# Performance work log

Measured on AMD Instinct MI355X. Metric: run time of the kernel, lower is better.

## Reference

```python
import jax, jax.numpy as jnp
import numpy as np

EMBED_DIM = 2048
NUM_HEADS = 32
HEAD_DIM = EMBED_DIM // NUM_HEADS  # 64
SCALE = HEAD_DIM ** -0.5


def setup_inputs() -> dict:
    key = jax.random.key(0)
    k1, k2, k3, k4, k5 = jax.random.split(key, 5)
    B, S, D = 1, 2048, EMBED_DIM
    return {
        "hidden_states": jax.random.normal(k1, (B, S, D), jnp.float32),
        "w_qkv": jax.random.normal(k2, (3 * D, D), jnp.float32) * (D ** -0.5),
        "b_qkv": jax.random.normal(k3, (3 * D,), jnp.float32) * 0.02,
        "w_out": jax.random.normal(k4, (D, D), jnp.float32) * (D ** -0.5),
        "b_out": jax.random.normal(k5, (D,), jnp.float32) * 0.02,
    }


def reference(hidden_states, w_qkv, b_qkv, w_out, b_out):
    B, S, D = hidden_states.shape
    H, Hd = NUM_HEADS, HEAD_DIM
    # fused QKV projection: [B,S,3D]
    qkv = jnp.einsum("bsd,ed->bse", hidden_states, w_qkv) + b_qkv
    q, k, v = jnp.split(qkv, 3, axis=-1)
    # [B,H,S,Hd]
    q = q.reshape(B, S, H, Hd).transpose(0, 2, 1, 3)
    k = k.reshape(B, S, H, Hd).transpose(0, 2, 1, 3)
    v = v.reshape(B, S, H, Hd).transpose(0, 2, 1, 3)
    scores = jnp.einsum("bhqd,bhkd->bhqk", q, k) * SCALE
    causal = jnp.tril(jnp.ones((S, S), bool))  # [S,S]
    scores = jnp.where(causal, scores, jnp.finfo(scores.dtype).min)
    probs = jax.nn.softmax(scores, axis=-1)
    attn = jnp.einsum("bhqk,bhkd->bhqd", probs, v)
    attn = attn.transpose(0, 2, 1, 3).reshape(B, S, D)
    return jnp.einsum("bsd,ed->bse", attn, w_out) + b_out
```

## Files before the change

kernel.cpp:

```cpp
#include <hip/hip_runtime.h>
#include <hip/hip_bf16.h>

typedef __bf16 bf16;
typedef __attribute__((ext_vector_type(8))) __bf16 bf16x8;
typedef __attribute__((ext_vector_type(4))) float f32x4;

#define S_LEN 2048
#define DM 2048
#define NH 32
#define HD 64
#define QKV_LD 6144
#define SCALE2 0.18033688011112042f
#define DEFER_THR 8.0f

__device__ __forceinline__ float fast_exp2(float x) {
  return __builtin_amdgcn_exp2f(x);
}

__device__ __forceinline__ void gload_lds16(const bf16* g, const bf16* l) {
  __builtin_amdgcn_global_load_lds(
      (const __attribute__((address_space(1))) void*)(uintptr_t)g,
      (__attribute__((address_space(3))) void*)(uint32_t)(uintptr_t)l,
      16, 0, 0);
}

template <int N>
__device__ __forceinline__ void waitcnt_vm() {
  if constexpr (N == 0)      asm volatile("s_waitcnt vmcnt(0)" ::: "memory");
  else if constexpr (N == 4) asm volatile("s_waitcnt vmcnt(4)" ::: "memory");
  else if constexpr (N == 5) asm volatile("s_waitcnt vmcnt(5)" ::: "memory");
  else if constexpr (N == 6) asm volatile("s_waitcnt vmcnt(6)" ::: "memory");
  else if constexpr (N == 7) asm volatile("s_waitcnt vmcnt(7)" ::: "memory");
  else if constexpr (N == 8) asm volatile("s_waitcnt vmcnt(8)" ::: "memory");
  else static_assert(N == 0, "add vmcnt case");
}

template <int CTRL>
__device__ __forceinline__ float fdpp(float x) {
  return __builtin_bit_cast(float,
      __builtin_amdgcn_update_dpp(0, __builtin_bit_cast(int, x), CTRL, 0xF, 0xF, true));
}
__device__ __forceinline__ float red16_max(float x) {
  x = fmaxf(x, fdpp<0xB1>(x));
  x = fmaxf(x, fdpp<0x4E>(x));
  x = fmaxf(x, fdpp<0x141>(x));
  x = fmaxf(x, fdpp<0x140>(x));
  return x;
}
__device__ __forceinline__ float red16_sum(float x) {
  x += fdpp<0xB1>(x);
  x += fdpp<0x4E>(x);
  x += fdpp<0x141>(x);
  x += fdpp<0x140>(x);
  return x;
}

__global__ __launch_bounds__(256) void cvt3_f32_bf16(
    const float* __restrict__ s0, bf16* __restrict__ d0, const int n0,
    const float* __restrict__ s1, bf16* __restrict__ d1, const int n1,
    const float* __restrict__ s2, bf16* __restrict__ d2, const int n2)
{
  const int total = n0 + n1 + n2;
  const int stride = gridDim.x * blockDim.x;
  for (int i = blockIdx.x * blockDim.x + threadIdx.x; i < total; i += stride) {
    const float* s; bf16* d; int j = i;
    if (j < n0)            { s = s0; d = d0; }
    else if (j - n0 < n1)  { s = s1; d = d1; j -= n0; }
    else                   { s = s2; d = d2; j -= n0 + n1; }
    const f32x4 a = *(const f32x4*)(s + (size_t)j * 8);
    const f32x4 b = *(const f32x4*)(s + (size_t)j * 8 + 4);
    bf16x8 r;
    r[0] = (bf16)a[0]; r[1] = (bf16)a[1]; r[2] = (bf16)a[2]; r[3] = (bf16)a[3];
    r[4] = (bf16)b[0]; r[5] = (bf16)b[1]; r[6] = (bf16)b[2]; r[7] = (bf16)b[3];
    *(bf16x8*)(d + (size_t)j * 8) = r;
  }
}

template <int BM, int BN, int WRN, int WCN, int NT, int MINW, typename TO>
__global__ __launch_bounds__(NT, MINW) void gemm_pipe(
    const bf16* __restrict__ A, const bf16* __restrict__ W,
    const float* __restrict__ bias, TO* __restrict__ C,
    const int M, const int N, const int K)
{
  constexpr int WM = BM / WRN, WN = BN / WCN;
  constexpr int MI = WM / 16, NI = WN / 16;
  constexpr int CA = (BM * 64 * 2) / (NT * 16);
  constexpr int CB = (BN * 64 * 2) / (NT * 16);
  constexpr int BUFE = (BM + BN) * 64;
  __shared__ __align__(16) bf16 lds[2 * BUFE];
  const int tid  = threadIdx.x;
  const int lane = tid & 63;
  const int wid  = tid >> 6;
  const int wr = wid / WCN, wc = wid % WCN;
  const int row0 = blockIdx.y * BM, col0 = blockIdx.x * BN;
  const int lq = lane & 15, seg = lane >> 4;

  const f32x4 fz = {0.f, 0.f, 0.f, 0.f};
  f32x4 acc[MI][NI];
#pragma unroll
  for (int i = 0; i < MI; ++i)
#pragma unroll
    for (int j = 0; j < NI; ++j) acc[i][j] = fz;

  auto stage = [&](const int kt, const int b) {
    const int k0 = kt << 6;
    bf16* Ab = lds + b * BUFE;
    bf16* Bb = Ab + BM * 64;
#pragma unroll
    for (int c = 0; c < CA; ++c) {
      const int off16 = c * NT + tid;
      const int row = off16 >> 3;
      const int ch  = (off16 & 7) ^ (row & 7);
      gload_lds16(A + (size_t)(row0 + row) * K + k0 + (ch << 3),
                  Ab + (size_t)(c * NT + (wid << 6)) * 8);
    }
#pragma unroll
    for (int c = 0; c < CB; ++c) {
      const int off16 = c * NT + tid;
      const int row = off16 >> 3;
      const int ch  = (off16 & 7) ^ (row & 7);
      gload_lds16(W + (size_t)(col0 + row) * K + k0 + (ch << 3),
                  Bb + (size_t)(c * NT + (wid << 6)) * 8);
    }
  };

  const int nt = K >> 6;
  stage(0, 0);

  for (int t = 0; t < nt; ++t) {
    asm volatile("" ::: "memory");
    __builtin_amdgcn_s_barrier();
    asm volatile("" ::: "memory");
    if (t + 1 < nt) {
      stage(t + 1, (t + 1) & 1);
      waitcnt_vm<CA + CB>();
    } else {
      waitcnt_vm<0>();
    }
    __builtin_amdgcn_s_barrier();
    asm volatile("" ::: "memory");

    const bf16* Ab = lds + (t & 1) * BUFE;
    const bf16* Bb = Ab + BM * 64;
#pragma unroll
    for (int kk = 0; kk < 2; ++kk) {
      bf16x8 af[MI], bfr[NI];
#pragma unroll
      for (int i = 0; i < MI; ++i) {
        const int row = wr * WM + (i << 4) + lq;
        af[i] = *(const bf16x8*)(Ab + row * 64 +
                 ((((kk << 2) + seg) ^ (row & 7)) << 3));
      }
#pragma unroll
      for (int j = 0; j < NI; ++j) {
        const int row = wc * WN + (j << 4) + lq;
        bfr[j] = *(const bf16x8*)(Bb + row * 64 +
                 ((((kk << 2) + seg) ^ (row & 7)) << 3));
      }
      __builtin_amdgcn_s_setprio(1);
#pragma unroll
      for (int i = 0; i < MI; ++i)
#pragma unroll
        for (int j = 0; j < NI; ++j)
          acc[i][j] = __builtin_amdgcn_mfma_f32_16x16x32_bf16(af[i], bfr[j], acc[i][j], 0, 0, 0);
      __builtin_amdgcn_s_setprio(0);
    }
  }

#pragma unroll
  for (int j = 0; j < NI; ++j) {
    const int col = col0 + wc * WN + (j << 4) + lq;
    const float bv = bias[col];
#pragma unroll
    for (int i = 0; i < MI; ++i) {
      const int rbase = row0 + wr * WM + (i << 4) + (seg << 2);
#pragma unroll
      for (int r = 0; r < 4; ++r)
        C[(size_t)(rbase + r) * N + col] = (TO)(acc[i][j][r] + bv);
    }
  }
}

struct QTile {
  bf16x8 qf[2];
  f32x4  o[4];
  float  m[4], l[4];
};

__device__ __forceinline__ void qtile_init(QTile& st, const bf16* Qg,
                                           const int lq, const int seg) {
  const bf16x8 r0 = *(const bf16x8*)(Qg + (size_t)lq * QKV_LD + seg * 8);
  const bf16x8 r1 = *(const bf16x8*)(Qg + (size_t)lq * QKV_LD + 32 + seg * 8);
#pragma unroll
  for (int j = 0; j < 8; ++j) {
    st.qf[0][j] = (bf16)((float)r0[j] * SCALE2);
    st.qf[1][j] = (bf16)((float)r1[j] * SCALE2);
  }
  const f32x4 fz = {0.f, 0.f, 0.f, 0.f};
#pragma unroll
  for (int r = 0; r < 4; ++r) { st.o[r] = fz; st.m[r] = -1e30f; st.l[r] = 0.f; }
}

__device__ __forceinline__ void qtile_step(
    QTile& st, const int qb, const int nt,
    const int ws, const int lq, const int seg,
    const bf16 (&Ks)[64][64], const bf16 (&Vt)[64][64], bf16 (&Psw)[16][64])
{
  const f32x4 fz = {0.f, 0.f, 0.f, 0.f};
  f32x4 s[4];
  __builtin_amdgcn_s_setprio(1);
#pragma unroll
  for (int ct = 0; ct < 4; ++ct) {
    s[ct] = fz;
#pragma unroll
    for (int ks = 0; ks < 2; ++ks) {
      const int blk = ((ks << 2) + seg) ^ (lq & 7);
      const bf16x8 kf = *(const bf16x8*)(&Ks[(ct << 4) + lq][blk << 3]);
      s[ct] = __builtin_amdgcn_mfma_f32_16x16x32_bf16(st.qf[ks], kf, s[ct], 0, 0, 0);
    }
  }
  __builtin_amdgcn_s_setprio(0);

  if (nt == qb) {
#pragma unroll
    for (int ct = 0; ct < 4; ++ct) {
      const int key = (nt << 6) + (ct << 4) + lq;
#pragma unroll
      for (int r = 0; r < 4; ++r) {
        const int qrow = (qb << 6) + (ws << 4) + (seg << 2) + r;
        if (key > qrow) s[ct][r] = -1e30f;
      }
    }
  }

#pragma unroll
  for (int r = 0; r < 4; ++r) {
    float tm = fmaxf(fmaxf(s[0][r], s[1][r]), fmaxf(s[2][r], s[3][r]));
    tm = red16_max(tm);
    if (tm > st.m[r] + DEFER_THR) {
      const float sc = fast_exp2(st.m[r] - tm);
      st.m[r] = tm;
      st.l[r] *= sc;
#pragma unroll
      for (int dt = 0; dt < 4; ++dt) st.o[dt][r] *= sc;
    }
    float rs = 0.f;
#pragma unroll
    for (int ct = 0; ct < 4; ++ct) {
      const float p = fast_exp2(s[ct][r] - st.m[r]);
      s[ct][r] = p;
      rs += p;
    }
    rs = red16_sum(rs);
    st.l[r] += rs;
  }

#pragma unroll
  for (int ct = 0; ct < 4; ++ct)
#pragma unroll
    for (int r = 0; r < 4; ++r) {
      const int q = (seg << 2) + r;
      const int colp = ((ct << 4) + lq) ^ ((q & 7) << 3);
      Psw[q][colp] = (bf16)s[ct][r];
    }

  __builtin_amdgcn_s_setprio(1);
#pragma unroll
  for (int ks = 0; ks < 2; ++ks) {
    const int blkp = ((ks << 2) + seg) ^ (lq & 7);
    const bf16x8 af = *(const bf16x8*)(&Psw[lq][blkp << 3]);
#pragma unroll
    for (int dt = 0; dt < 4; ++dt) {
      const int xv = (lq & 7) ^ (((dt << 1) + (lq >> 3)) & 7);
      const int blkv = ((ks << 2) + seg) ^ xv;
      const bf16x8 bv = *(const bf16x8*)(&Vt[(dt << 4) + lq][blkv << 3]);
      st.o[dt] = __builtin_amdgcn_mfma_f32_16x16x32_bf16(af, bv, st.o[dt], 0, 0, 0);
    }
  }
  __builtin_amdgcn_s_setprio(0);
}

__device__ __forceinline__ void qtile_store(
    const QTile& st, bf16* __restrict__ out, const int qb, const int h,
    const int ws, const int lq, const int seg)
{
  float rinv[4];
#pragma unroll
  for (int r = 0; r < 4; ++r) rinv[r] = 1.f / st.l[r];
#pragma unroll
  for (int dt = 0; dt < 4; ++dt)
#pragma unroll
    for (int r = 0; r < 4; ++r) {
      const int qrow = (qb << 6) + (ws << 4) + (seg << 2) + r;
      out[(size_t)qrow * DM + h * HD + (dt << 4) + lq] =
          (bf16)(st.o[dt][r] * rinv[r]);
    }
}

__global__ __launch_bounds__(512, 4) void attn_flash(
    const bf16* __restrict__ qkv, bf16* __restrict__ out)
{
  __shared__ __align__(16) bf16 Ks[2][64][64];
  __shared__ __align__(16) bf16 Vt[2][64][64];
  __shared__ __align__(16) bf16 Ps[8][16][64];
  const int bid = blockIdx.x;
  const int xcd = bid & 7, idx = bid >> 3;
  const int h   = (xcd << 2) | (idx >> 4);
  const int qbA = idx & 15;
  const int qbB = 31 - qbA;
  const int tid = threadIdx.x;
  const int lane = tid & 63, wid = tid >> 6;
  const int lq = lane & 15, seg = lane >> 4;
  const int myqb = (wid < 4) ? qbA : qbB;
  const int ws   = wid & 3;

  const bf16* Kg = qkv + DM + h * HD;
  const bf16* Vg = qkv + 2 * DM + h * HD;

  QTile st;
  qtile_init(st, qkv + (size_t)(myqb * 64 + ws * 16) * QKV_LD + h * HD, lq, seg);

  const int srow = tid >> 3, sch = tid & 7;

  {
    const bf16x8 k0 = *(const bf16x8*)(Kg + (size_t)srow * QKV_LD + (sch << 3));
    const bf16x8 v0 = *(const bf16x8*)(Vg + (size_t)srow * QKV_LD + (sch << 3));
    *(bf16x8*)(&Ks[0][srow][(sch ^ (srow & 7)) << 3]) = k0;
#pragma unroll
    for (int j = 0; j < 8; ++j)
      Vt[0][(sch << 3) + j][srow ^ ((j ^ sch) << 3)] = v0[j];
  }
  __syncthreads();

  for (int nt = 0; nt <= qbB; ++nt) {
    bf16x8 kr, vr;
    if (nt < qbB) {
      const int row = ((nt + 1) << 6) + srow;
      kr = *(const bf16x8*)(Kg + (size_t)row * QKV_LD + (sch << 3));
      vr = *(const bf16x8*)(Vg + (size_t)row * QKV_LD + (sch << 3));
    }

    if (nt <= myqb)
      qtile_step(st, myqb, nt, ws, lq, seg, Ks[nt & 1], Vt[nt & 1], Ps[wid]);

    if (nt < qbB) {
      const int b = (nt + 1) & 1;
      *(bf16x8*)(&Ks[b][srow][(sch ^ (srow & 7)) << 3]) = kr;
#pragma unroll
      for (int j = 0; j < 8; ++j)
        Vt[b][(sch << 3) + j][srow ^ ((j ^ sch) << 3)] = vr[j];
    }
    __syncthreads();
  }

  qtile_store(st, out, myqb, h, ws, lq, seg);
}

extern "C" void kernel_launch(void* const* d_in, const int* in_sizes, int n_in,
                              void* d_out, int out_size, void* d_ws, size_t ws_size,
                              hipStream_t stream) {
  (void)in_sizes; (void)n_in; (void)out_size; (void)ws_size;
  const float* hidden = (const float*)d_in[0];
  const float* w_qkv  = (const float*)d_in[1];
  const float* b_qkv  = (const float*)d_in[2];
  const float* w_out  = (const float*)d_in[3];
  const float* b_out  = (const float*)d_in[4];
  float* out = (float*)d_out;

  bf16* qkvbuf  = (bf16*)d_ws;
  bf16* attnbuf = qkvbuf  + (size_t)S_LEN * (3 * DM);
  bf16* hidb    = attnbuf + (size_t)S_LEN * DM;
  bf16* wqkvb   = hidb    + (size_t)S_LEN * DM;
  bf16* woutb   = wqkvb   + (size_t)(3 * DM) * DM;

  dim3 blk(256);
  cvt3_f32_bf16<<<dim3(2048), blk, 0, stream>>>(
      hidden, hidb, (S_LEN * DM) / 8,
      w_qkv, wqkvb, (3 * DM * DM) / 8,
      w_out, woutb, (DM * DM) / 8);
  gemm_pipe<128, 192, 2, 4, 512, 4, bf16><<<dim3(32, 16), dim3(512), 0, stream>>>(
      hidb, wqkvb, b_qkv, qkvbuf, S_LEN, 3 * DM, DM);
  attn_flash<<<dim3(512), dim3(512), 0, stream>>>(qkvbuf, attnbuf);
  gemm_pipe<64, 128, 1, 4, 256, 2, float><<<dim3(16, 32), dim3(256), 0, stream>>>(
      attnbuf, woutb, b_out, out, S_LEN, DM, DM);
}
```

Baseline: 147.9 us.

## Split paired causal q-block attention blocks into one q-block per workgroup

The attention kernel previously paired a short and a long causal query block (qb and 31-qb) in one 512-thread workgroup so that per-block work was balanced. It now launches 1024 workgroups of 256 threads, each handling a single query block, with blocks ordered longest-first, and each thread loads two K/V rows per tile. This removes the idle waves in the paired scheme (the short half sat waiting at barriers while the long half finished) and relies on the hardware scheduler plus descending order for load balance. In exchange, each K/V tile is loaded from global memory once per query block instead of once per pair, so K/V traffic roughly doubles.

```diff
diff --git a/kernel.cpp b/kernel.cpp
--- a/kernel.cpp
+++ b/kernel.cpp
@@ -297,63 +297,68 @@
     }
 }
 
-__global__ __launch_bounds__(512, 4) void attn_flash(
+__global__ __launch_bounds__(256, 4) void attn_flash(
     const bf16* __restrict__ qkv, bf16* __restrict__ out)
 {
   __shared__ __align__(16) bf16 Ks[2][64][64];
   __shared__ __align__(16) bf16 Vt[2][64][64];
-  __shared__ __align__(16) bf16 Ps[8][16][64];
+  __shared__ __align__(16) bf16 Ps[4][16][64];
   const int bid = blockIdx.x;
   const int xcd = bid & 7, idx = bid >> 3;
-  const int h   = (xcd << 2) | (idx >> 4);
-  const int qbA = idx & 15;
-  const int qbB = 31 - qbA;
+  const int h   = (xcd << 2) | (idx >> 5);
+  const int qb  = 31 - (idx & 31);
   const int tid = threadIdx.x;
   const int lane = tid & 63, wid = tid >> 6;
   const int lq = lane & 15, seg = lane >> 4;
-  const int myqb = (wid < 4) ? qbA : qbB;
-  const int ws   = wid & 3;
 
   const bf16* Kg = qkv + DM + h * HD;
   const bf16* Vg = qkv + 2 * DM + h * HD;
 
   QTile st;
-  qtile_init(st, qkv + (size_t)(myqb * 64 + ws * 16) * QKV_LD + h * HD, lq, seg);
+  qtile_init(st, qkv + (size_t)(qb * 64 + wid * 16) * QKV_LD + h * HD, lq, seg);
 
   const int srow = tid >> 3, sch = tid & 7;
 
-  {
-    const bf16x8 k0 = *(const bf16x8*)(Kg + (size_t)srow * QKV_LD + (sch << 3));
-    const bf16x8 v0 = *(const bf16x8*)(Vg + (size_t)srow * QKV_LD + (sch << 3));
-    *(bf16x8*)(&Ks[0][srow][(sch ^ (srow & 7)) << 3]) = k0;
+#pragma unroll
+  for (int c = 0; c < 2; ++c) {
+    const int row = (c << 5) + srow;
+    const bf16x8 k0 = *(const bf16x8*)(Kg + (size_t)row * QKV_LD + (sch << 3));
+    const bf16x8 v0 = *(const bf16x8*)(Vg + (size_t)row * QKV_LD + (sch << 3));
+    *(bf16x8*)(&Ks[0][row][(sch ^ (row & 7)) << 3]) = k0;
 #pragma unroll
     for (int j = 0; j < 8; ++j)
-      Vt[0][(sch << 3) + j][srow ^ ((j ^ sch) << 3)] = v0[j];
+      Vt[0][(sch << 3) + j][row ^ ((j ^ sch) << 3)] = v0[j];
   }
   __syncthreads();
 
-  for (int nt = 0; nt <= qbB; ++nt) {
-    bf16x8 kr, vr;
-    if (nt < qbB) {
-      const int row = ((nt + 1) << 6) + srow;
-      kr = *(const bf16x8*)(Kg + (size_t)row * QKV_LD + (sch << 3));
-      vr = *(const bf16x8*)(Vg + (size_t)row * QKV_LD + (sch << 3));
-    }
-
-    if (nt <= myqb)
-      qtile_step(st, myqb, nt, ws, lq, seg, Ks[nt & 1], Vt[nt & 1], Ps[wid]);
-
-    if (nt < qbB) {
+  for (int nt = 0; nt <= qb; ++nt) {
+    bf16x8 kr[2], vr[2];
+    if (nt < qb) {
+#pragma unroll
+      for (int c = 0; c < 2; ++c) {
+        const int row = ((nt + 1) << 6) + (c << 5) + srow;
+        kr[c] = *(const bf16x8*)(Kg + (size_t)row * QKV_LD + (sch << 3));
+        vr[c] = *(const bf16x8*)(Vg + (size_t)row * QKV_LD + (sch << 3));
+      }
+    }
+
+    qtile_step(st, qb, nt, wid, lq, seg, Ks[nt & 1], Vt[nt & 1], Ps[wid]);
+
+    if (nt < qb) {
       const int b = (nt + 1) & 1;
-      *(bf16x8*)(&Ks[b][srow][(sch ^ (srow & 7)) << 3]) = kr;
-#pragma unroll
-      for (int j = 0; j < 8; ++j)
-        Vt[b][(sch << 3) + j][srow ^ ((j ^ sch) << 3)] = vr[j];
+#pragma unroll
+      for (int c = 0; c < 2; ++c) {
+        const int row = (c << 5) + srow;
+        *(bf16x8*)(&Ks[b][row][(sch ^ (row & 7)) << 3]) = kr[c];
+#pragma unroll
+        for (int j = 0; j < 8; ++j)
+          Vt[b][(sch << 3) + j][row ^ ((j ^ sch) << 3)] = vr[c][j];
+      }
     }
     __syncthreads();
   }
 
-  qtile_store(st, out, myqb, h, ws, lq, seg);
+  qtile_store(st, out, qb, h, wid, lq, seg);
 }
 
 extern "C" void kernel_launch(void* const* d_in, const int* in_sizes, int n_in,
@@ -380,7 +385,7 @@
       w_out, woutb, (DM * DM) / 8);
   gemm_pipe<128, 192, 2, 4, 512, 4, bf16><<<dim3(32, 16), dim3(512), 0, stream>>>(
       hidb, wqkvb, b_qkv, qkvbuf, S_LEN, 3 * DM, DM);
-  attn_flash<<<dim3(512), dim3(512), 0, stream>>>(qkvbuf, attnbuf);
+  attn_flash<<<dim3(1024), dim3(256), 0, stream>>>(qkvbuf, attnbuf);
   gemm_pipe<64, 128, 1, 4, 256, 2, float><<<dim3(16, 32), dim3(256), 0, stream>>>(
       attnbuf, woutb, b_out, out, S_LEN, DM, DM);
 }
```

After: 177.6 us. 1.2x slower.

## Split long causal query tile across warp groups with LSE merge

Applied to the files above, without the earlier changes.

The attention kernel pairs a short query tile (qbA) with a long one (qbB). Previously the qbA waves sat idle once their causal range ended. Now, after finishing qbA, those waves process the upper half of qbB's key range, using a second double-buffered K/V staging set. The partial softmax states are then merged through shared memory with a log-sum-exp rescale. This balances work so every block runs 17 iterations instead of up to 32, at the cost of extra LDS, more registers for a second query tile state, and a merge step.

```diff
diff --git a/kernel.cpp b/kernel.cpp
--- a/kernel.cpp
+++ b/kernel.cpp
@@ -300,8 +300,10 @@
 __global__ __launch_bounds__(512, 4) void attn_flash(
     const bf16* __restrict__ qkv, bf16* __restrict__ out)
 {
-  __shared__ __align__(16) bf16 Ks[2][64][64];
-  __shared__ __align__(16) bf16 Vt[2][64][64];
+  __shared__ __align__(16) bf16 Ks0[2][64][64];
+  __shared__ __align__(16) bf16 Vt0[2][64][64];
+  __shared__ __align__(16) bf16 Ks1[2][64][64];
+  __shared__ __align__(16) bf16 Vt1[2][64][64];
   __shared__ __align__(16) bf16 Ps[8][16][64];
   const int bid = blockIdx.x;
   const int xcd = bid & 7, idx = bid >> 3;
@@ -311,49 +313,108 @@
   const int tid = threadIdx.x;
   const int lane = tid & 63, wid = tid >> 6;
   const int lq = lane & 15, seg = lane >> 4;
-  const int myqb = (wid < 4) ? qbA : qbB;
+  const bool isA = (wid < 4);
   const int ws   = wid & 3;
 
   const bf16* Kg = qkv + DM + h * HD;
   const bf16* Vg = qkv + 2 * DM + h * HD;
 
-  QTile st;
-  qtile_init(st, qkv + (size_t)(myqb * 64 + ws * 16) * QKV_LD + h * HD, lq, seg);
+  QTile stP, stS;
+  qtile_init(stP, qkv + (size_t)((isA ? qbA : qbB) * 64 + ws * 16) * QKV_LD + h * HD,
+             lq, seg);
+  if (isA)
+    qtile_init(stS, qkv + (size_t)(qbB * 64 + ws * 16) * QKV_LD + h * HD, lq, seg);
 
   const int srow = tid >> 3, sch = tid & 7;
 
   {
     const bf16x8 k0 = *(const bf16x8*)(Kg + (size_t)srow * QKV_LD + (sch << 3));
     const bf16x8 v0 = *(const bf16x8*)(Vg + (size_t)srow * QKV_LD + (sch << 3));
-    *(bf16x8*)(&Ks[0][srow][(sch ^ (srow & 7)) << 3]) = k0;
+    *(bf16x8*)(&Ks0[0][srow][(sch ^ (srow & 7)) << 3]) = k0;
 #pragma unroll
     for (int j = 0; j < 8; ++j)
-      Vt[0][(sch << 3) + j][srow ^ ((j ^ sch) << 3)] = v0[j];
+      Vt0[0][(sch << 3) + j][srow ^ ((j ^ sch) << 3)] = v0[j];
   }
   __syncthreads();
 
-  for (int nt = 0; nt <= qbB; ++nt) {
-    bf16x8 kr, vr;
-    if (nt < qbB) {
-      const int row = ((nt + 1) << 6) + srow;
-      kr = *(const bf16x8*)(Kg + (size_t)row * QKV_LD + (sch << 3));
-      vr = *(const bf16x8*)(Vg + (size_t)row * QKV_LD + (sch << 3));
-    }
-
-    if (nt <= myqb)
-      qtile_step(st, myqb, nt, ws, lq, seg, Ks[nt & 1], Vt[nt & 1], Ps[wid]);
-
-    if (nt < qbB) {
-      const int b = (nt + 1) & 1;
-      *(bf16x8*)(&Ks[b][srow][(sch ^ (srow & 7)) << 3]) = kr;
+  for (int t = 0; t <= 16; ++t) {
+    const bool st0 = (t < 16);
+    const bool st1 = (t >= qbA && t <= 14);
+    bf16x8 kr0, vr0, kr1, vr1;
+    if (st0) {
+      const int row = ((t + 1) << 6) + srow;
+      kr0 = *(const bf16x8*)(Kg + (size_t)row * QKV_LD + (sch << 3));
+      vr0 = *(const bf16x8*)(Vg + (size_t)row * QKV_LD + (sch << 3));
+    }
+    if (st1) {
+      const int row = ((17 + (t - qbA)) << 6) + srow;
+      kr1 = *(const bf16x8*)(Kg + (size_t)row * QKV_LD + (sch << 3));
+      vr1 = *(const bf16x8*)(Vg + (size_t)row * QKV_LD + (sch << 3));
+    }
+
+    if (isA) {
+      if (t <= qbA) {
+        qtile_step(stP, qbA, t, ws, lq, seg, Ks0[t & 1], Vt0[t & 1], Ps[wid]);
+      } else {
+        const int nt1 = 16 + t - qbA;
+        if (nt1 <= qbB)
+          qtile_step(stS, qbB, nt1, ws, lq, seg,
+                     Ks1[(t - qbA - 1) & 1], Vt1[(t - qbA - 1) & 1], Ps[wid]);
+      }
+    } else {
+      qtile_step(stP, qbB, t, ws, lq, seg, Ks0[t & 1], Vt0[t & 1], Ps[wid]);
+    }
+
+    if (st0) {
+      const int b = (t + 1) & 1;
+      *(bf16x8*)(&Ks0[b][srow][(sch ^ (srow & 7)) << 3]) = kr0;
 #pragma unroll
       for (int j = 0; j < 8; ++j)
-        Vt[b][(sch << 3) + j][srow ^ ((j ^ sch) << 3)] = vr[j];
+        Vt0[b][(sch << 3) + j][srow ^ ((j ^ sch) << 3)] = vr0[j];
+    }
+    if (st1) {
+      const int b = (t - qbA) & 1;
+      *(bf16x8*)(&Ks1[b][srow][(sch ^ (srow & 7)) << 3]) = kr1;
+#pragma unroll
+      for (int j = 0; j < 8; ++j)
+        Vt1[b][(sch << 3) + j][srow ^ ((j ^ sch) << 3)] = vr1[j];
     }
     __syncthreads();
   }
 
-  qtile_store(st, out, myqb, h, ws, lq, seg);
+  float* so  = (float*)&Ks0[0][0][0];
+  float* sml = (float*)&Vt0[0][0][0];
+  const int sbase = (ws << 6) + lane;
+  if (isA) {
+    qtile_store(stP, out, qbA, h, ws, lq, seg);
+#pragma unroll
+    for (int dt = 0; dt < 4; ++dt)
+#pragma unroll
+      for (int r = 0; r < 4; ++r)
+        so[sbase * 16 + (dt << 2) + r] = stS.o[dt][r];
+#pragma unroll
+    for (int r = 0; r < 4; ++r) {
+      sml[sbase * 8 + r]     = stS.m[r];
+      sml[sbase * 8 + 4 + r] = stS.l[r];
+    }
+  }
+  __syncthreads();
+  if (!isA) {
+#pragma unroll
+    for (int r = 0; r < 4; ++r) {
+      const float pm = sml[sbase * 8 + r];
+      const float pl = sml[sbase * 8 + 4 + r];
+      const float mf = fmaxf(stP.m[r], pm);
+      const float a  = fast_exp2(stP.m[r] - mf);
+      const float b  = fast_exp2(pm - mf);
+      stP.m[r] = mf;
+      stP.l[r] = stP.l[r] * a + pl * b;
+#pragma unroll
+      for (int dt = 0; dt < 4; ++dt)
+        stP.o[dt][r] = stP.o[dt][r] * a + so[sbase * 16 + (dt << 2) + r] * b;
+    }
+    qtile_store(stP, out, qbB, h, ws, lq, seg);
+  }
 }
 
 extern "C" void kernel_launch(void* const* d_in, const int* in_sizes, int n_in,
```

Result: slower. 245.1 us (+65.8%).
